# Optimization experiments

Hardware: AMD Instinct MI355X
Metric: run time of the kernel (lower is better)

## Reference

```python
import jax, jax.numpy as jnp
import numpy as np

BATCH, SEQ, INPUT, HIDDEN = 256, 512, 128, 256

def setup_inputs() -> dict:
    key = jax.random.key(0)
    ks = jax.random.split(key, 7)
    s = 1.0 / np.sqrt(INPUT + HIDDEN)
    return {
        "X": jax.random.normal(ks[0], (BATCH, SEQ, INPUT), dtype=jnp.float32),
        "W_z": jax.random.normal(ks[1], (HIDDEN, INPUT + HIDDEN), dtype=jnp.float32) * s,
        "b_z": jax.random.normal(ks[2], (HIDDEN,), dtype=jnp.float32) * s,
        "W_r": jax.random.normal(ks[3], (HIDDEN, INPUT + HIDDEN), dtype=jnp.float32) * s,
        "b_r": jax.random.normal(ks[4], (HIDDEN,), dtype=jnp.float32) * s,
        "W_c": jax.random.normal(ks[5], (HIDDEN, INPUT + HIDDEN), dtype=jnp.float32) * s,
        "b_c": jax.random.normal(ks[6], (HIDDEN,), dtype=jnp.float32) * s,
    }

def reference(X, W_z, b_z, W_r, b_r, W_c, b_c):
    # X: [batch, seq, input] -> scan over time (seq, batch, input)
    Xt = jnp.transpose(X, (1, 0, 2))
    h0 = jnp.zeros((X.shape[0], HIDDEN), dtype=X.dtype)

    def step(h, x):
        hx = jnp.concatenate([h, x], axis=1)          # [B, H+I] (cat order: h then x)
        z = jax.nn.sigmoid(hx @ W_z.T + b_z)          # update gate
        r = jax.nn.sigmoid(hx @ W_r.T + b_r)          # reset gate
        rhx = jnp.concatenate([r * h, x], axis=1)
        cand = jnp.tanh(rhx @ W_c.T + b_c)            # candidate state
        h_new = (1.0 - z) * h + z * cand
        return h_new, h_new

    _, h_history = jax.lax.scan(step, h0, Xt)
    return h_history  # [seq, batch, hidden]
```

## Files before the change

kernel.cpp:

```cpp
#include <hip/hip_runtime.h>
#include <hip/hip_bf16.h>


typedef float f32x4 __attribute__((ext_vector_type(4)));
typedef short s16x8 __attribute__((ext_vector_type(8)));

#define SEQ 512
#define NB  256
#define NI  128
#define NH  256
#define WROW 384
#define GX_BYTES ((size_t)201326592)

static __device__ inline float bf2f(unsigned short s) {
    unsigned u = ((unsigned)s) << 16;
    return __builtin_bit_cast(float, u);
}
static __device__ inline unsigned pkbf(float a, float b) {
    __hip_bfloat162 h = __float22bfloat162_rn(make_float2(a, b));
    unsigned r;
    __builtin_memcpy(&r, &h, 4);
    return r;
}
static __device__ inline s16x8 pk8(f32x4 f0, f32x4 f1) {
    uint4 u;
    u.x = pkbf(f0[0], f0[1]);
    u.y = pkbf(f0[2], f0[3]);
    u.z = pkbf(f1[0], f1[1]);
    u.w = pkbf(f1[2], f1[3]);
    return __builtin_bit_cast(s16x8, u);
}
static __device__ inline float fexp2(float x) {
#if __has_builtin(__builtin_amdgcn_exp2f)
    return __builtin_amdgcn_exp2f(x);
#else
    return exp2f(x);
#endif
}
static __device__ inline float frcp(float x) {
#if __has_builtin(__builtin_amdgcn_rcpf)
    return __builtin_amdgcn_rcpf(x);
#else
    return 1.0f / x;
#endif
}
static __device__ inline float sigm(float x)  { return frcp(1.0f + fexp2(-1.44269504f * x)); }
static __device__ inline float tanh_(float x) { return 1.0f - 2.0f * frcp(1.0f + fexp2(2.88539008f * x)); }

static __device__ inline void lds_barrier() {
    asm volatile("s_waitcnt lgkmcnt(0)\n\ts_barrier" ::: "memory");
}

__global__ __launch_bounds__(256, 1) void gru_xpre(
    const float* __restrict__ X,
    const float* __restrict__ Wz, const float* __restrict__ bz,
    const float* __restrict__ Wr, const float* __restrict__ br,
    const float* __restrict__ Wc, const float* __restrict__ bc,
    unsigned short* __restrict__ Gx)
{
    __shared__ unsigned short x_lds[32768];
    const int tid  = threadIdx.x;
    const int t    = blockIdx.x;
    const int l    = tid & 63;
    const int v    = tid >> 6;
    const int quad = l >> 4;
    const int n    = l & 15;

    for (int i = tid; i < 4096; i += 256) {
        int row = i >> 4, c = i & 15;
        const float* src = X + (size_t)(row * SEQ + t) * NI + c * 8;
        f32x4 f0 = *(const f32x4*)(src);
        f32x4 f1 = *(const f32x4*)(src + 4);
        *(s16x8*)(&x_lds[row * 128 + ((c ^ (row & 15)) << 3)]) = pk8(f0, f1);
    }

    const float* Wp[3] = {Wz, Wr, Wc};
    const float* bp[3] = {bz, br, bc};
    s16x8 Bf[3][4][4];
    float bias[3][4];
#pragma unroll
    for (int g = 0; g < 3; ++g) {
#pragma unroll
        for (int tt = 0; tt < 4; ++tt) {
            int j = v * 64 + tt * 16 + n;
            bias[g][tt] = bp[g][j];
#pragma unroll
            for (int kt = 0; kt < 4; ++kt) {
                const float* src = Wp[g] + j * WROW + 256 + kt * 32 + quad * 8;
                f32x4 f0 = *(const f32x4*)(src);
                f32x4 f1 = *(const f32x4*)(src + 4);
                Bf[g][tt][kt] = pk8(f0, f1);
            }
        }
    }
    __syncthreads();

    const int rowA = l & 15;
#pragma unroll 1
    for (int mt = 0; mt < 16; ++mt) {
        f32x4 acc[3][4];
        f32x4 z4 = {0.f, 0.f, 0.f, 0.f};
#pragma unroll
        for (int g = 0; g < 3; ++g)
#pragma unroll
            for (int tt = 0; tt < 4; ++tt) acc[g][tt] = z4;

#pragma unroll
        for (int kt = 0; kt < 4; ++kt) {
            int row = mt * 16 + rowA;
            s16x8 a = *(const s16x8*)(&x_lds[row * 128 + (((kt * 4 + quad) ^ rowA) << 3)]);
#pragma unroll
            for (int g = 0; g < 3; ++g)
#pragma unroll
                for (int tt = 0; tt < 4; ++tt)
                    acc[g][tt] = __builtin_amdgcn_mfma_f32_16x16x32_bf16(a, Bf[g][tt][kt], acc[g][tt], 0, 0, 0);
        }

#pragma unroll
        for (int g = 0; g < 3; ++g)
#pragma unroll
            for (int tt = 0; tt < 4; ++tt) {
                float b = bias[g][tt];
                uint2 d;
                d.x = pkbf(acc[g][tt][0] + b, acc[g][tt][1] + b);
                d.y = pkbf(acc[g][tt][2] + b, acc[g][tt][3] + b);
                int chunk = (((t * 16 + mt) * 4 + v) * 3 + g) * 4 + tt;
                *(uint2*)((char*)Gx + (size_t)chunk * 512 + l * 8) = d;
            }
    }
}

__global__ __launch_bounds__(512, 2) void gru_seq(
    const float* __restrict__ Wz, const float* __restrict__ Wr, const float* __restrict__ Wc,
    const unsigned short* __restrict__ Gx,
    float* __restrict__ out)
{
    __shared__ unsigned short wc_lds[32768];
    __shared__ unsigned short h_lds[16][264];
    __shared__ unsigned short rh_lds[16][264];

    const int tid  = threadIdx.x;
    const int wg   = blockIdx.x;
    const int l    = tid & 63;
    const int w    = tid >> 6;
    const int quad = l >> 4;
    const int n    = l & 15;
    const int rowA = n;

    const float* Wp2[2] = {Wz, Wr};
    s16x8 Wf[2][2][8];
#pragma unroll
    for (int g = 0; g < 2; ++g)
#pragma unroll
        for (int tt = 0; tt < 2; ++tt)
#pragma unroll
            for (int kt = 0; kt < 8; ++kt) {
                int j = w * 32 + tt * 16 + n;
                const float* src = Wp2[g] + j * WROW + kt * 32 + quad * 8;
                f32x4 f0 = *(const f32x4*)(src);
                f32x4 f1 = *(const f32x4*)(src + 4);
                Wf[g][tt][kt] = pk8(f0, f1);
            }

    s16x8 Wcr[2][4];
#pragma unroll
    for (int tt = 0; tt < 2; ++tt)
#pragma unroll
        for (int kt = 0; kt < 4; ++kt) {
            int j = w * 32 + tt * 16 + n;
            const float* src = Wc + j * WROW + kt * 32 + quad * 8;
            f32x4 f0 = *(const f32x4*)(src);
            f32x4 f1 = *(const f32x4*)(src + 4);
            Wcr[tt][kt] = pk8(f0, f1);
        }

    for (int idx = tid; idx < 4096; idx += 512) {
        int fr = idx >> 6, ln = idx & 63;
        int jb = fr >> 2, ktm = fr & 3;
        int j = jb * 16 + (ln & 15);
        int k = (ktm + 4) * 32 + (ln >> 4) * 8;
        const float* src = Wc + j * WROW + k;
        f32x4 f0 = *(const f32x4*)(src);
        f32x4 f1 = *(const f32x4*)(src + 4);
        *(s16x8*)(&wc_lds[idx * 8]) = pk8(f0, f1);
    }

    {
        unsigned short* hz = &h_lds[0][0];
        for (int i = tid; i < 16 * 264; i += 512) hz[i] = 0;
    }
    float hreg[2][4];
#pragma unroll
    for (int tt = 0; tt < 2; ++tt)
#pragma unroll
        for (int r = 0; r < 4; ++r) hreg[tt][r] = 0.0f;
    __syncthreads();

    const char* gxbase = (const char*)Gx
        + (size_t)(((wg * 4 + (w >> 1)) * 12 + (w & 1) * 2) * 512) + l * 8;
    float* outp = out + (size_t)(wg * 16 + quad * 4) * 256 + w * 32 + n;
    const f32x4 z4 = {0.f, 0.f, 0.f, 0.f};

    uint2 ga[6];
#pragma unroll
    for (int i = 0; i < 6; ++i)
        ga[i] = *(const uint2*)(gxbase + (i >> 1) * 2048 + (i & 1) * 512);

#pragma unroll 1
    for (int t = 0; t < SEQ; ++t) {
        const char* gbn = gxbase + (size_t)(t + 1 < SEQ ? t + 1 : t) * 393216;

        f32x4 accZ[2], accR[2];
#pragma unroll
        for (int tt = 0; tt < 2; ++tt) { accZ[tt] = z4; accR[tt] = z4; }
#pragma unroll
        for (int kt = 0; kt < 8; ++kt) {
            s16x8 a = *(const s16x8*)(&h_lds[rowA][kt * 32 + quad * 8]);
#pragma unroll
            for (int tt = 0; tt < 2; ++tt) {
                accZ[tt] = __builtin_amdgcn_mfma_f32_16x16x32_bf16(a, Wf[0][tt][kt], accZ[tt], 0, 0, 0);
                accR[tt] = __builtin_amdgcn_mfma_f32_16x16x32_bf16(a, Wf[1][tt][kt], accR[tt], 0, 0, 0);
            }
        }

        float zs[2][4];
        {
            float gzf[2][4], grf[2][4];
#pragma unroll
            for (int tt = 0; tt < 2; ++tt) {
                uint2 gz = ga[tt], gr = ga[2 + tt];
                gzf[tt][0] = bf2f((unsigned short)(gz.x & 0xffffu));
                gzf[tt][1] = bf2f((unsigned short)(gz.x >> 16));
                gzf[tt][2] = bf2f((unsigned short)(gz.y & 0xffffu));
                gzf[tt][3] = bf2f((unsigned short)(gz.y >> 16));
                grf[tt][0] = bf2f((unsigned short)(gr.x & 0xffffu));
                grf[tt][1] = bf2f((unsigned short)(gr.x >> 16));
                grf[tt][2] = bf2f((unsigned short)(gr.y & 0xffffu));
                grf[tt][3] = bf2f((unsigned short)(gr.y >> 16));
            }
#pragma unroll
            for (int i = 0; i < 4; ++i)
                ga[i] = *(const uint2*)(gbn + (i >> 1) * 2048 + (i & 1) * 512);
#pragma unroll
            for (int tt = 0; tt < 2; ++tt) {
                float rh[4];
#pragma unroll
                for (int r = 0; r < 4; ++r) {
                    float zv = sigm(accZ[tt][r] + gzf[tt][r]);
                    float rv = sigm(accR[tt][r] + grf[tt][r]);
                    zs[tt][r] = zv;
                    rh[r] = rv * hreg[tt][r];
                }
                unsigned pa = pkbf(rh[0], rh[1]);
                unsigned pb = pkbf(rh[2], rh[3]);
                const int col = w * 32 + tt * 16 + n;
                rh_lds[quad * 4 + 0][col] = (unsigned short)pa;
                rh_lds[quad * 4 + 1][col] = (unsigned short)(pa >> 16);
                rh_lds[quad * 4 + 2][col] = (unsigned short)pb;
                rh_lds[quad * 4 + 3][col] = (unsigned short)(pb >> 16);
            }
        }
        lds_barrier();

        f32x4 accC[2];
#pragma unroll
        for (int tt = 0; tt < 2; ++tt) accC[tt] = z4;
#pragma unroll
        for (int kt = 0; kt < 8; ++kt) {
            s16x8 a = *(const s16x8*)(&rh_lds[rowA][kt * 32 + quad * 8]);
#pragma unroll
            for (int tt = 0; tt < 2; ++tt) {
                s16x8 b = (kt < 4)
                    ? Wcr[tt][kt]
                    : *(const s16x8*)(&wc_lds[(((w * 2 + tt) * 4 + (kt - 4)) * 64 + l) * 8]);
                accC[tt] = __builtin_amdgcn_mfma_f32_16x16x32_bf16(a, b, accC[tt], 0, 0, 0);
            }
        }

        {
            float gcf[2][4];
#pragma unroll
            for (int tt = 0; tt < 2; ++tt) {
                uint2 gc = ga[4 + tt];
                gcf[tt][0] = bf2f((unsigned short)(gc.x & 0xffffu));
                gcf[tt][1] = bf2f((unsigned short)(gc.x >> 16));
                gcf[tt][2] = bf2f((unsigned short)(gc.y & 0xffffu));
                gcf[tt][3] = bf2f((unsigned short)(gc.y >> 16));
            }
#pragma unroll
            for (int i = 4; i < 6; ++i)
                ga[i] = *(const uint2*)(gbn + 4096 + (i & 1) * 512);
#pragma unroll
            for (int tt = 0; tt < 2; ++tt) {
                float hn4[4];
#pragma unroll
                for (int r = 0; r < 4; ++r) {
                    float cv = tanh_(accC[tt][r] + gcf[tt][r]);
                    float h  = hreg[tt][r];
                    float hn = fmaf(zs[tt][r], cv - h, h);
                    hreg[tt][r] = hn;
                    hn4[r] = hn;
                    outp[(size_t)t * 65536 + r * 256 + tt * 16] = hn;
                }
                unsigned pa = pkbf(hn4[0], hn4[1]);
                unsigned pb = pkbf(hn4[2], hn4[3]);
                const int col = w * 32 + tt * 16 + n;
                h_lds[quad * 4 + 0][col] = (unsigned short)pa;
                h_lds[quad * 4 + 1][col] = (unsigned short)(pa >> 16);
                h_lds[quad * 4 + 2][col] = (unsigned short)pb;
                h_lds[quad * 4 + 3][col] = (unsigned short)(pb >> 16);
            }
        }
        lds_barrier();
    }
}

__global__ __launch_bounds__(1024, 1) void gru_fallback(
    const float* __restrict__ X,
    const float* __restrict__ Wz, const float* __restrict__ bz,
    const float* __restrict__ Wr, const float* __restrict__ br,
    const float* __restrict__ Wc, const float* __restrict__ bc,
    float* __restrict__ out)
{
    __shared__ float h_s[16][257];
    __shared__ float rh_s[16][257];
    __shared__ float x_s[16][128];
    const int tid = threadIdx.x;
    const int wg = blockIdx.x, b0 = wg * 16;
    const int m = tid >> 6, jq = tid & 63;
    for (int i = tid; i < 16 * 257; i += 1024) (&h_s[0][0])[i] = 0.0f;
    __syncthreads();
    for (int t = 0; t < SEQ; ++t) {
        for (int i = tid; i < 2048; i += 1024) {
            int row = i >> 7, k = i & 127;
            x_s[row][k] = X[(size_t)((b0 + row) * SEQ + t) * NI + k];
        }
        __syncthreads();
        float zv[4];
        for (int jj = 0; jj < 4; ++jj) {
            int j = jj * 64 + jq;
            float az = bz[j], ar = br[j];
            for (int k = 0; k < 256; ++k) { float h = h_s[m][k]; az += h * Wz[j * WROW + k]; ar += h * Wr[j * WROW + k]; }
            for (int k = 0; k < 128; ++k) { float x = x_s[m][k]; az += x * Wz[j * WROW + 256 + k]; ar += x * Wr[j * WROW + 256 + k]; }
            float z = sigm(az), r = sigm(ar);
            zv[jj] = z;
            rh_s[m][j] = r * h_s[m][j];
        }
        __syncthreads();
        float hn[4];
        for (int jj = 0; jj < 4; ++jj) {
            int j = jj * 64 + jq;
            float ac = bc[j];
            for (int k = 0; k < 256; ++k) ac += rh_s[m][k] * Wc[j * WROW + k];
            for (int k = 0; k < 128; ++k) ac += x_s[m][k] * Wc[j * WROW + 256 + k];
            float c = tanh_(ac);
            float h = h_s[m][j];
            hn[jj] = fmaf(zv[jj], c - h, h);
        }
        __syncthreads();
        for (int jj = 0; jj < 4; ++jj) {
            int j = jj * 64 + jq;
            h_s[m][j] = hn[jj];
            out[(size_t)(t * 256 + b0 + m) * 256 + j] = hn[jj];
        }
        __syncthreads();
    }
}

extern "C" void kernel_launch(void* const* d_in, const int* in_sizes, int n_in,
                              void* d_out, int out_size, void* d_ws, size_t ws_size,
                              hipStream_t stream) {
    const float* X  = (const float*)d_in[0];
    const float* Wz = (const float*)d_in[1];
    const float* bz = (const float*)d_in[2];
    const float* Wr = (const float*)d_in[3];
    const float* br = (const float*)d_in[4];
    const float* Wc = (const float*)d_in[5];
    const float* bc = (const float*)d_in[6];
    float* out = (float*)d_out;

    if (ws_size >= GX_BYTES) {
        unsigned short* Gx = (unsigned short*)d_ws;
        gru_xpre<<<512, 256, 0, stream>>>(X, Wz, bz, Wr, br, Wc, bc, Gx);
        gru_seq<<<16, 512, 0, stream>>>(Wz, Wr, Wc, Gx, out);
    } else {
        gru_fallback<<<16, 1024, 0, stream>>>(X, Wz, bz, Wr, br, Wc, bc, out);
    }
}
```

Baseline: 1.169 ms.

## Prepack input weights for xpre, permute h/rh LDS rows, prioritize MFMA waves

```diff
diff --git a/kernel.cpp b/kernel.cpp
--- a/kernel.cpp
+++ b/kernel.cpp
@@ -11,6 +11,7 @@
 #define NH  256
 #define WROW 384
 #define GX_BYTES ((size_t)201326592)
+#define WTAB_BYTES ((size_t)196608)
 
 static __device__ inline float bf2f(unsigned short s) {
     unsigned u = ((unsigned)s) << 16;
@@ -51,7 +52,106 @@
     asm volatile("s_waitcnt lgkmcnt(0)\n\ts_barrier" ::: "memory");
 }
 
+static __device__ inline int prow(int m) {
+    return 2 * (m >> 2) + (m & 1) + 8 * ((m >> 1) & 1);
+}
+
+__global__ __launch_bounds__(256, 1) void gru_wprep(
+    const float* __restrict__ Wz, const float* __restrict__ Wr, const float* __restrict__ Wc,
+    unsigned short* __restrict__ wtab)
+{
+    int task = blockIdx.x * 256 + threadIdx.x;
+    int l  = task & 63;
+    int fr = task >> 6;
+    int v  = fr / 48;
+    int f  = fr - v * 48;
+    int g  = f >> 4, tt = (f >> 2) & 3, kt = f & 3;
+    const float* Wp = (g == 0) ? Wz : (g == 1) ? Wr : Wc;
+    int j = v * 64 + tt * 16 + (l & 15);
+    const float* src = Wp + (size_t)j * WROW + 256 + kt * 32 + (l >> 4) * 8;
+    f32x4 f0 = *(const f32x4*)src;
+    f32x4 f1 = *(const f32x4*)(src + 4);
+    *(s16x8*)(wtab + (size_t)task * 8) = pk8(f0, f1);
+}
+
 __global__ __launch_bounds__(256, 1) void gru_xpre(
+    const float* __restrict__ X,
+    const float* __restrict__ bz, const float* __restrict__ br, const float* __restrict__ bc,
+    const unsigned short* __restrict__ wtab,
+    unsigned short* __restrict__ Gx)
+{
+    __shared__ unsigned short x_lds[32768];
+    const int tid  = threadIdx.x;
+    const int t    = blockIdx.x;
+    const int l    = tid & 63;
+    const int v    = tid >> 6;
+    const int quad = l >> 4;
+    const int n    = l & 15;
+
+    for (int i = tid; i < 4096; i += 256) {
+        int row = i >> 4, c = i & 15;
+        const float* src = X + (size_t)(row * SEQ + t) * NI + c * 8;
+        f32x4 f0 = *(const f32x4*)(src);
+        f32x4 f1 = *(const f32x4*)(src + 4);
+        *(s16x8*)(&x_lds[row * 128 + ((c ^ (row & 15)) << 3)]) = pk8(f0, f1);
+    }
+
+    s16x8 Bf[3][4][4];
+    float bias[3][4];
+    {
+        const unsigned short* wt = wtab + ((size_t)v * 48 * 64 + l) * 8;
+#pragma unroll
+        for (int g = 0; g < 3; ++g)
+#pragma unroll
+            for (int tt = 0; tt < 4; ++tt)
+#pragma unroll
+                for (int kt = 0; kt < 4; ++kt)
+                    Bf[g][tt][kt] = *(const s16x8*)(wt + (size_t)(g * 16 + tt * 4 + kt) * 64 * 8);
+        const float* bp[3] = {bz, br, bc};
+#pragma unroll
+        for (int g = 0; g < 3; ++g)
+#pragma unroll
+            for (int tt = 0; tt < 4; ++tt)
+                bias[g][tt] = bp[g][v * 64 + tt * 16 + n];
+    }
+    __syncthreads();
+
+    const int rowA = l & 15;
+#pragma unroll 1
+    for (int mt = 0; mt < 16; ++mt) {
+        f32x4 acc[3][4];
+        f32x4 z4 = {0.f, 0.f, 0.f, 0.f};
+#pragma unroll
+        for (int g = 0; g < 3; ++g)
+#pragma unroll
+            for (int tt = 0; tt < 4; ++tt) acc[g][tt] = z4;
+
+#pragma unroll
+        for (int kt = 0; kt < 4; ++kt) {
+            int row = mt * 16 + rowA;
+            s16x8 a = *(const s16x8*)(&x_lds[row * 128 + (((kt * 4 + quad) ^ rowA) << 3)]);
+#pragma unroll
+            for (int g = 0; g < 3; ++g)
+#pragma unroll
+                for (int tt = 0; tt < 4; ++tt)
+                    acc[g][tt] = __builtin_amdgcn_mfma_f32_16x16x32_bf16(a, Bf[g][tt][kt], acc[g][tt], 0, 0, 0);
+        }
+
+#pragma unroll
+        for (int g = 0; g < 3; ++g)
+#pragma unroll
+            for (int tt = 0; tt < 4; ++tt) {
+                float b = bias[g][tt];
+                uint2 d;
+                d.x = pkbf(acc[g][tt][0] + b, acc[g][tt][1] + b);
+                d.y = pkbf(acc[g][tt][2] + b, acc[g][tt][3] + b);
+                int chunk = (((t * 16 + mt) * 4 + v) * 3 + g) * 4 + tt;
+                *(uint2*)((char*)Gx + (size_t)chunk * 512 + l * 8) = d;
+            }
+    }
+}
+
+__global__ __launch_bounds__(256, 1) void gru_xpre_gather(
     const float* __restrict__ X,
     const float* __restrict__ Wz, const float* __restrict__ bz,
     const float* __restrict__ Wr, const float* __restrict__ br,
@@ -145,7 +245,7 @@
     const int w    = tid >> 6;
     const int quad = l >> 4;
     const int n    = l & 15;
-    const int rowA = n;
+    const int rowR = prow(n);
 
     const float* Wp2[2] = {Wz, Wr};
     s16x8 Wf[2][2][8];
@@ -201,6 +301,9 @@
     float* outp = out + (size_t)(wg * 16 + quad * 4) * 256 + w * 32 + n;
     const f32x4 z4 = {0.f, 0.f, 0.f, 0.f};
 
+    int wr0 = prow(quad * 4 + 0), wr1 = prow(quad * 4 + 1);
+    int wr2 = prow(quad * 4 + 2), wr3 = prow(quad * 4 + 3);
+
     uint2 ga[6];
 #pragma unroll
     for (int i = 0; i < 6; ++i)
@@ -213,15 +316,17 @@
         f32x4 accZ[2], accR[2];
 #pragma unroll
         for (int tt = 0; tt < 2; ++tt) { accZ[tt] = z4; accR[tt] = z4; }
+        __builtin_amdgcn_s_setprio(1);
 #pragma unroll
         for (int kt = 0; kt < 8; ++kt) {
-            s16x8 a = *(const s16x8*)(&h_lds[rowA][kt * 32 + quad * 8]);
+            s16x8 a = *(const s16x8*)(&h_lds[rowR][kt * 32 + quad * 8]);
 #pragma unroll
             for (int tt = 0; tt < 2; ++tt) {
                 accZ[tt] = __builtin_amdgcn_mfma_f32_16x16x32_bf16(a, Wf[0][tt][kt], accZ[tt], 0, 0, 0);
                 accR[tt] = __builtin_amdgcn_mfma_f32_16x16x32_bf16(a, Wf[1][tt][kt], accR[tt], 0, 0, 0);
             }
         }
+        __builtin_amdgcn_s_setprio(0);
 
         float zs[2][4];
         {
@@ -254,10 +359,10 @@
                 unsigned pa = pkbf(rh[0], rh[1]);
                 unsigned pb = pkbf(rh[2], rh[3]);
                 const int col = w * 32 + tt * 16 + n;
-                rh_lds[quad * 4 + 0][col] = (unsigned short)pa;
-                rh_lds[quad * 4 + 1][col] = (unsigned short)(pa >> 16);
-                rh_lds[quad * 4 + 2][col] = (unsigned short)pb;
-                rh_lds[quad * 4 + 3][col] = (unsigned short)(pb >> 16);
+                rh_lds[wr0][col] = (unsigned short)pa;
+                rh_lds[wr1][col] = (unsigned short)(pa >> 16);
+                rh_lds[wr2][col] = (unsigned short)pb;
+                rh_lds[wr3][col] = (unsigned short)(pb >> 16);
             }
         }
         lds_barrier();
@@ -265,9 +370,10 @@
         f32x4 accC[2];
 #pragma unroll
         for (int tt = 0; tt < 2; ++tt) accC[tt] = z4;
+        __builtin_amdgcn_s_setprio(1);
 #pragma unroll
         for (int kt = 0; kt < 8; ++kt) {
-            s16x8 a = *(const s16x8*)(&rh_lds[rowA][kt * 32 + quad * 8]);
+            s16x8 a = *(const s16x8*)(&rh_lds[rowR][kt * 32 + quad * 8]);
 #pragma unroll
             for (int tt = 0; tt < 2; ++tt) {
                 s16x8 b = (kt < 4)
@@ -276,6 +382,7 @@
                 accC[tt] = __builtin_amdgcn_mfma_f32_16x16x32_bf16(a, b, accC[tt], 0, 0, 0);
             }
         }
+        __builtin_amdgcn_s_setprio(0);
 
         {
             float gcf[2][4];
@@ -290,6 +397,7 @@
 #pragma unroll
             for (int i = 4; i < 6; ++i)
                 ga[i] = *(const uint2*)(gbn + 4096 + (i & 1) * 512);
+            float* op = outp + (size_t)t * 65536;
 #pragma unroll
             for (int tt = 0; tt < 2; ++tt) {
                 float hn4[4];
@@ -300,15 +408,15 @@
                     float hn = fmaf(zs[tt][r], cv - h, h);
                     hreg[tt][r] = hn;
                     hn4[r] = hn;
-                    outp[(size_t)t * 65536 + r * 256 + tt * 16] = hn;
+                    op[r * 256 + tt * 16] = hn;
                 }
                 unsigned pa = pkbf(hn4[0], hn4[1]);
                 unsigned pb = pkbf(hn4[2], hn4[3]);
                 const int col = w * 32 + tt * 16 + n;
-                h_lds[quad * 4 + 0][col] = (unsigned short)pa;
-                h_lds[quad * 4 + 1][col] = (unsigned short)(pa >> 16);
-                h_lds[quad * 4 + 2][col] = (unsigned short)pb;
-                h_lds[quad * 4 + 3][col] = (unsigned short)(pb >> 16);
+                h_lds[wr0][col] = (unsigned short)pa;
+                h_lds[wr1][col] = (unsigned short)(pa >> 16);
+                h_lds[wr2][col] = (unsigned short)pb;
+                h_lds[wr3][col] = (unsigned short)(pb >> 16);
             }
         }
         lds_barrier();
@@ -379,9 +487,15 @@
     const float* bc = (const float*)d_in[6];
     float* out = (float*)d_out;
 
-    if (ws_size >= GX_BYTES) {
+    if (ws_size >= GX_BYTES + WTAB_BYTES) {
+        unsigned short* Gx   = (unsigned short*)d_ws;
+        unsigned short* wtab = (unsigned short*)((char*)d_ws + GX_BYTES);
+        gru_wprep<<<48, 256, 0, stream>>>(Wz, Wr, Wc, wtab);
+        gru_xpre<<<512, 256, 0, stream>>>(X, bz, br, bc, wtab, Gx);
+        gru_seq<<<16, 512, 0, stream>>>(Wz, Wr, Wc, Gx, out);
+    } else if (ws_size >= GX_BYTES) {
         unsigned short* Gx = (unsigned short*)d_ws;
-        gru_xpre<<<512, 256, 0, stream>>>(X, Wz, bz, Wr, br, Wc, bc, Gx);
+        gru_xpre_gather<<<512, 256, 0, stream>>>(X, Wz, bz, Wr, br, Wc, bc, Gx);
         gru_seq<<<16, 512, 0, stream>>>(Wz, Wr, Wc, Gx, out);
     } else {
         gru_fallback<<<16, 1024, 0, stream>>>(X, Wz, bz, Wr, br, Wc, bc, out);
```

Result: slower. 1.196 ms (+2.3%).
